# Kernel optimization log

Hardware: AMD Instinct MI355X
Metric: run time of the kernel (lower is better)

## Reference

```python
import jax, jax.numpy as jnp
import numpy as np

N_PROD, N_CUST = 100000, 50000
HID, OUT = 128, 64
E_PP, E_PC, E_LB = 800000, 800000, 400000


def sage(x_src, x_dst, src, dst, Wl, bl, Wr, n_dst):
    # PyG SAGEConv (mean aggr): lin_l(mean_{j->i} x_j) + lin_r(x_i); bias on lin_l only
    msg = x_src[src]                                             # [E, d] gather
    s = jax.ops.segment_sum(msg, dst, num_segments=n_dst)        # [n_dst, d]
    cnt = jax.ops.segment_sum(jnp.ones((src.shape[0],), x_src.dtype), dst, num_segments=n_dst)
    mean = s / jnp.maximum(cnt, 1.0)[:, None]
    return mean @ Wl.T + bl + x_dst @ Wr.T


def setup_inputs() -> dict:
    key = jax.random.key(0)
    ks = iter(jax.random.split(key, 40))

    def lin_w(i, o):
        return (jax.random.normal(next(ks), (o, i), jnp.float32) / np.sqrt(i))

    inp = {}
    inp['x_product'] = jax.random.normal(next(ks), (N_PROD, HID), jnp.float32)
    inp['x_customer'] = jax.random.normal(next(ks), (N_CUST, HID), jnp.float32)
    inp['ei_pp'] = jax.random.randint(next(ks), (2, E_PP), 0, N_PROD)
    src_pc = jax.random.randint(next(ks), (1, E_PC), 0, N_PROD)
    dst_pc = jax.random.randint(next(ks), (1, E_PC), 0, N_CUST)
    inp['ei_pc'] = jnp.concatenate([src_pc, dst_pc], axis=0)
    row = jax.random.randint(next(ks), (1, E_LB), 0, N_CUST)
    col = jax.random.randint(next(ks), (1, E_LB), 0, N_PROD)
    inp['edge_label_index'] = jnp.concatenate([row, col], axis=0)

    # ItemGNNEncoder params
    inp['it_W1l'], inp['it_W1r'] = lin_w(HID, HID), lin_w(HID, HID)
    inp['it_b1'] = jnp.zeros((HID,), jnp.float32)
    inp['it_W2l'], inp['it_W2r'] = lin_w(HID, HID), lin_w(HID, HID)
    inp['it_b2'] = jnp.zeros((HID,), jnp.float32)
    inp['it_Wlin'] = lin_w(HID, OUT)
    inp['it_blin'] = jnp.zeros((OUT,), jnp.float32)
    # UserGNNEncoder params
    inp['us_W1l'], inp['us_W1r'] = lin_w(HID, HID), lin_w(HID, HID)
    inp['us_b1'] = jnp.zeros((HID,), jnp.float32)
    inp['us_W2l'], inp['us_W2r'] = lin_w(HID, HID), lin_w(HID, HID)
    inp['us_b2'] = jnp.zeros((HID,), jnp.float32)
    inp['us_W3l'], inp['us_W3r'] = lin_w(HID, HID), lin_w(HID, HID)
    inp['us_b3'] = jnp.zeros((HID,), jnp.float32)
    inp['us_Wlin'] = lin_w(HID, OUT)
    inp['us_blin'] = jnp.zeros((OUT,), jnp.float32)
    # EdgeDecoder params
    inp['de_W1'] = lin_w(2 * OUT, OUT)
    inp['de_b1'] = jnp.zeros((OUT,), jnp.float32)
    inp['de_W2'] = lin_w(OUT, 1)
    inp['de_b2'] = jnp.zeros((1,), jnp.float32)
    return inp


def reference(x_product, x_customer, ei_pp, ei_pc, edge_label_index,
              it_W1l, it_b1, it_W1r, it_W2l, it_b2, it_W2r, it_Wlin, it_blin,
              us_W1l, us_b1, us_W1r, us_W2l, us_b2, us_W2r, us_W3l, us_b3, us_W3r,
              us_Wlin, us_blin, de_W1, de_b1, de_W2, de_b2):
    pp_s, pp_d = ei_pp[0], ei_pp[1]
    pc_s, pc_d = ei_pc[0], ei_pc[1]

    # ItemGNNEncoder on product-product metapath
    p = jax.nn.relu(sage(x_product, x_product, pp_s, pp_d, it_W1l, it_b1, it_W1r, N_PROD))
    p = jax.nn.relu(sage(p, p, pp_s, pp_d, it_W2l, it_b2, it_W2r, N_PROD))
    z_prod = p @ it_Wlin.T + it_blin                              # [N_PROD, OUT]

    # UserGNNEncoder
    px = jax.nn.relu(sage(x_product, x_product, pp_s, pp_d, us_W1l, us_b1, us_W1r, N_PROD))
    cx = jax.nn.relu(sage(x_product, x_customer, pc_s, pc_d, us_W2l, us_b2, us_W2r, N_CUST))
    cx = jax.nn.relu(sage(px, cx, pc_s, pc_d, us_W3l, us_b3, us_W3r, N_CUST))
    z_cust = cx @ us_Wlin.T + us_blin                             # [N_CUST, OUT]

    # EdgeDecoder: gather-concat-MLP
    row, col = edge_label_index[0], edge_label_index[1]
    z = jnp.concatenate([z_cust[row], z_prod[col]], axis=-1)      # [E_LB, 2*OUT]
    z = jax.nn.relu(z @ de_W1.T + de_b1)
    return z @ de_W2.T + de_b2                                    # [E_LB, 1]
```

## Files before the change

kernel.cpp:

```cpp
#include <hip/hip_runtime.h>
#include <hip/hip_bf16.h>

#define HID   128
#define OUTD  64
#define NPROD 100000
#define NCUST 50000
#define EPP   800000
#define EPC   800000
#define ELB   400000
#define NBK   391
#define EBLK  4096
#define RCAP3 512
#define BCAP3 2560
#define CPADN 400
#define NB3   392
#define NCAST 6250

typedef __bf16 bf16x8 __attribute__((ext_vector_type(8)));
typedef float  f32x4  __attribute__((ext_vector_type(4)));
typedef unsigned short u16;
typedef unsigned int u32;

__device__ __forceinline__ float b2f(u16 u) {
  unsigned int v = ((unsigned int)u) << 16;
  float f; __builtin_memcpy(&f, &v, 4); return f;
}
__device__ __forceinline__ u16 f2b(float f) {
  __hip_bfloat16 h = __float2bfloat16(f);
  u16 u; __builtin_memcpy(&u, &h, 2); return u;
}

union Pack8 { u16 u[8]; int4 v; };

__device__ __forceinline__ int sidx(int row, int chunk) {
  return row * HID + ((chunk ^ (row & 15)) << 3);
}
__device__ __forceinline__ int sidx64(int row, int chunk) {
  return row * 64 + ((chunk ^ (row & 7)) << 3);
}

#define NJOBS 13
struct CastJobs { const float* src[NJOBS]; int n8[NJOBS]; };

__global__ __launch_bounds__(256) void k_prep(const int* __restrict__ ei_pp,
                                              const int* __restrict__ ei_pc,
                                              int* __restrict__ bfill_pp,
                                              int* __restrict__ bfill_pc,
                                              u32* __restrict__ bss_pp,
                                              u32* __restrict__ bss_pc,
                                              const float* __restrict__ x_prod,
                                              u16* __restrict__ XPB,
                                              CastJobs jobs,
                                              u16* __restrict__ wbuf) {
  __shared__ int lcnt[NBK], lstart[NBK], lfill[NBK], gbase[NBK];
  __shared__ u32 spay[EBLK];
  __shared__ u16 sbk[EBLK];
  __shared__ int wtot[4];
  const int t = threadIdx.x;
  int bid = blockIdx.x;

  if (bid >= NB3) {
    bid -= NB3;
    if (bid < NCAST) {
      int i = bid * 256 + t;
      float4 a = ((const float4*)x_prod)[2 * i];
      float4 b = ((const float4*)x_prod)[2 * i + 1];
      Pack8 p;
      p.u[0] = f2b(a.x); p.u[1] = f2b(a.y); p.u[2] = f2b(a.z); p.u[3] = f2b(a.w);
      p.u[4] = f2b(b.x); p.u[5] = f2b(b.y); p.u[6] = f2b(b.z); p.u[7] = f2b(b.w);
      ((int4*)XPB)[i] = p.v;
      return;
    }
    bid -= NCAST;
    int job = bid >> 3;
    int idx = (bid & 7) * 256 + t;
    int off8 = (job < 10) ? job * 2048 : 10 * 2048 + (job - 10) * 1024;
    if (idx >= jobs.n8[job]) return;
    const float* s = jobs.src[job];
    float4 a = ((const float4*)s)[2 * idx];
    float4 b = ((const float4*)s)[2 * idx + 1];
    Pack8 p;
    p.u[0] = f2b(a.x); p.u[1] = f2b(a.y); p.u[2] = f2b(a.z); p.u[3] = f2b(a.w);
    p.u[4] = f2b(b.x); p.u[5] = f2b(b.y); p.u[6] = f2b(b.z); p.u[7] = f2b(b.w);
    ((int4*)wbuf)[off8 + idx] = p.v;
    return;
  }

  const int lane = t & 63, wv = t >> 6;
  int xcc; asm("s_getreg_b32 %0, hwreg(HW_REG_XCC_ID)" : "=s"(xcc));
  const int rep = xcc & 7;
  const int NBLK_PP = (EPP + EBLK - 1) / EBLK;
  const bool isPP = bid < NBLK_PP;
  const int* ei = isPP ? ei_pp : ei_pc;
  const int E  = isPP ? EPP : EPC;
  const int SH = isPP ? 8 : 7;
  int* bfill = isPP ? bfill_pp : bfill_pc;
  u32* bss   = isPP ? bss_pp : bss_pc;
  const int base = (isPP ? bid : bid - NBLK_PP) * EBLK;
  const int n = min(EBLK, E - base);

  for (int j = t; j < NBK; j += 256) { lcnt[j] = 0; lfill[j] = 0; }
  __syncthreads();

  u32 pay[16]; int bk[16];
  const int e0 = t * 16;
  const int* srcp = ei + base;
  const int* dstp = ei + E + base;
  #pragma unroll
  for (int i = 0; i < 16; ++i) bk[i] = -1;
  if (e0 < n) {
    #pragma unroll
    for (int i = 0; i < 4; ++i) {
      int4 s4 = *(const int4*)(srcp + e0 + i * 4);
      int4 d4 = *(const int4*)(dstp + e0 + i * 4);
      int ss[4] = {s4.x, s4.y, s4.z, s4.w};
      int dd[4] = {d4.x, d4.y, d4.z, d4.w};
      #pragma unroll
      for (int j = 0; j < 4; ++j) {
        int b = dd[j] >> SH;
        bk[i * 4 + j] = b;
        pay[i * 4 + j] = ((u32)ss[j] << SH) | (u32)(dd[j] & ((1 << SH) - 1));
        atomicAdd(&lcnt[b], 1);
      }
    }
  }
  __syncthreads();
  {
    int a0 = (2 * t < NBK) ? lcnt[2 * t] : 0;
    int a1 = (2 * t + 1 < NBK) ? lcnt[2 * t + 1] : 0;
    int s = a0 + a1;
    #pragma unroll
    for (int d = 1; d < 64; d <<= 1) {
      int u = __shfl_up(s, d, 64);
      if (lane >= d) s += u;
    }
    if (lane == 63) wtot[wv] = s;
    __syncthreads();
    int wpre = 0;
    for (int w = 0; w < wv; ++w) wpre += wtot[w];
    int excl = s + wpre - (a0 + a1);
    if (2 * t < NBK) lstart[2 * t] = excl;
    if (2 * t + 1 < NBK) lstart[2 * t + 1] = excl + a0;
  }
  __syncthreads();
  for (int b = t; b < NBK; b += 256) {
    int c = lcnt[b];
    gbase[b] = c ? atomicAdd(&bfill[(rep * CPADN + b) << 4], c) : 0;
  }
  #pragma unroll
  for (int i = 0; i < 16; ++i) {
    if (bk[i] >= 0) {
      int pos = lstart[bk[i]] + atomicAdd(&lfill[bk[i]], 1);
      spay[pos] = pay[i];
      sbk[pos] = (u16)bk[i];
    }
  }
  __syncthreads();
  for (int i = t; i < n; i += 256) {
    int b = sbk[i];
    int slot = gbase[b] + (i - lstart[b]);
    if (slot < RCAP3)
      bss[(b * 8 + rep) * RCAP3 + slot] = spay[i];
  }
}

__global__ __launch_bounds__(256) void k_bsort2(const u32* __restrict__ bss_pp,
                                                const int* __restrict__ bfill_pp,
                                                const u32* __restrict__ bss_pc,
                                                const int* __restrict__ bfill_pc,
                                                int* __restrict__ gctr,
                                                int* __restrict__ esrc_pp,
                                                int* __restrict__ start_pp,
                                                int* __restrict__ cnt_pp,
                                                int* __restrict__ esrc_pc,
                                                int* __restrict__ start_pc,
                                                int* __restrict__ cnt_pc) {
  __shared__ u32 pairs[BCAP3];
  __shared__ int outsrc[BCAP3];
  __shared__ int lcnt[256], lstart[256], lfill[256];
  __shared__ int sh_n, sh_base, rn[8], roff[8], wtot[4];
  const int tid = threadIdx.x;
  const int lane = tid & 63, wv = tid >> 6;
  const bool isPP = (int)blockIdx.x < NBK;
  const int b = isPP ? (int)blockIdx.x : (int)blockIdx.x - NBK;
  const int K   = isPP ? 256 : 128;
  const int SHL = isPP ? 8 : 7;
  const u32* bss   = isPP ? bss_pp : bss_pc;
  const int* bfill = isPP ? bfill_pp : bfill_pc;
  int* gc    = isPP ? gctr : gctr + 1;
  int* esrc  = isPP ? esrc_pp : esrc_pc;
  int* start = isPP ? start_pp : start_pc;
  int* cnt   = isPP ? cnt_pp : cnt_pc;
  const int n_nodes = isPP ? NPROD : NCUST;

  if (tid < 8) rn[tid] = min(bfill[(tid * CPADN + b) << 4], RCAP3);
  for (int j = tid; j < K; j += 256) { lcnt[j] = 0; lfill[j] = 0; }
  __syncthreads();
  if (tid == 0) {
    int run = 0;
    for (int r = 0; r < 8; ++r) {
      roff[r] = run;
      int m = min(rn[r], BCAP3 - run);
      rn[r] = m;
      run += m;
    }
    sh_n = run;
    sh_base = atomicAdd(gc, run);
  }
  __syncthreads();
  const int n = sh_n, base = sh_base;
  const int Km1 = K - 1;
  #pragma unroll
  for (int r = 0; r < 8; ++r) {
    int m = rn[r], o = roff[r];
    for (int i = tid; i < m; i += 256) {
      u32 p = bss[(b * 8 + r) * RCAP3 + i];
      pairs[o + i] = p;
      atomicAdd(&lcnt[p & Km1], 1);
    }
  }
  __syncthreads();
  {
    int a0 = (2 * tid < K) ? lcnt[2 * tid] : 0;
    int a1 = (2 * tid + 1 < K) ? lcnt[2 * tid + 1] : 0;
    int s = a0 + a1;
    #pragma unroll
    for (int d = 1; d < 64; d <<= 1) {
      int u = __shfl_up(s, d, 64);
      if (lane >= d) s += u;
    }
    if (lane == 63) wtot[wv] = s;
    __syncthreads();
    int wpre = 0;
    for (int w = 0; w < wv; ++w) wpre += wtot[w];
    int excl = s + wpre - (a0 + a1);
    if (2 * tid < K) lstart[2 * tid] = excl;
    if (2 * tid + 1 < K) lstart[2 * tid + 1] = excl + a0;
  }
  __syncthreads();
  for (int i = tid; i < n; i += 256) {
    u32 p = pairs[i];
    int ln = p & Km1;
    int pos = lstart[ln] + atomicAdd(&lfill[ln], 1);
    outsrc[pos] = (int)(p >> SHL);
  }
  __syncthreads();
  for (int i = tid; i < n; i += 256) esrc[base + i] = outsrc[i];
  const int nb0 = b * K;
  for (int j = tid; j < K; j += 256) {
    int g = nb0 + j;
    if (g < n_nodes) { start[g] = base + lstart[j]; cnt[g] = lcnt[j]; }
  }
}

__global__ __launch_bounds__(256) void k_agg2(const int* __restrict__ es_a,
                                              const int* __restrict__ st_a,
                                              const int* __restrict__ cn_a,
                                              const u16* __restrict__ xa,
                                              u16* __restrict__ oa, int na,
                                              const int* __restrict__ es_b,
                                              const int* __restrict__ st_b,
                                              const int* __restrict__ cn_b,
                                              const u16* __restrict__ xb,
                                              u16* __restrict__ ob, int nb, int blkA) {
  const int t = threadIdx.x;
  const bool A = (int)blockIdx.x < blkA;
  const int node = (A ? (int)blockIdx.x : (int)blockIdx.x - blkA) * 16 + (t >> 4);
  const int l16 = t & 15;
  const int q4  = t & 48;
  if (node >= (A ? na : nb)) return;
  const int* esrc  = A ? es_a : es_b;
  const u16* x     = A ? xa : xb;
  u16* outm        = A ? oa : ob;
  int s0 = (A ? st_a : st_b)[node];
  int c  = (A ? cn_a : cn_b)[node];
  float acc[8] = {0.f, 0.f, 0.f, 0.f, 0.f, 0.f, 0.f, 0.f};
  for (int j0 = 0; j0 < c; j0 += 16) {
    int nch = min(16, c - j0);
    int eid = (l16 < nch) ? esrc[s0 + j0 + l16] : 0;
    int k = 0;
    for (; k + 4 <= nch; k += 4) {
      int s0i = __shfl(eid, q4 + k, 64);
      int s1i = __shfl(eid, q4 + k + 1, 64);
      int s2i = __shfl(eid, q4 + k + 2, 64);
      int s3i = __shfl(eid, q4 + k + 3, 64);
      Pack8 p0, p1, p2, p3;
      p0.v = *(const int4*)(x + (size_t)s0i * HID + l16 * 8);
      p1.v = *(const int4*)(x + (size_t)s1i * HID + l16 * 8);
      p2.v = *(const int4*)(x + (size_t)s2i * HID + l16 * 8);
      p3.v = *(const int4*)(x + (size_t)s3i * HID + l16 * 8);
      #pragma unroll
      for (int u = 0; u < 8; ++u)
        acc[u] += (b2f(p0.u[u]) + b2f(p1.u[u])) + (b2f(p2.u[u]) + b2f(p3.u[u]));
    }
    for (; k < nch; ++k) {
      int s = __shfl(eid, q4 + k, 64);
      Pack8 p;
      p.v = *(const int4*)(x + (size_t)s * HID + l16 * 8);
      #pragma unroll
      for (int u = 0; u < 8; ++u) acc[u] += b2f(p.u[u]);
    }
  }
  float inv = 1.0f / (float)max(c, 1);
  Pack8 o;
  #pragma unroll
  for (int u = 0; u < 8; ++u) o.u[u] = f2b(acc[u] * inv);
  *(int4*)(outm + (size_t)node * HID + l16 * 8) = o.v;
}

__global__ __launch_bounds__(256) void k_lay1(
    const u16* __restrict__ cxA1, const u16* __restrict__ cxW1,
    const float* __restrict__ cxA2f, const u16* __restrict__ cxW2,
    const float* __restrict__ cxBias, u16* __restrict__ cxOut, int Mcx,
    const u16* __restrict__ A1, const u16* __restrict__ A2,
    const u16* __restrict__ Wa, const u16* __restrict__ Wb,
    const u16* __restrict__ Wc, const u16* __restrict__ Wd,
    const float* __restrict__ bias1, const float* __restrict__ bias2,
    u16* __restrict__ out1, u16* __restrict__ out2, int M2o,
    int blkCx) {
  __shared__ __align__(16) u16 sA1[64 * HID];
  __shared__ __align__(16) u16 sA2[64 * HID];
  __shared__ __align__(16) u16 sW[128 * HID];
  const int tid  = threadIdx.x;
  const int lane = tid & 63;
  const int wave = tid >> 6;
  const int q    = lane >> 4;
  const int r16  = lane & 15;
  const bool isCx = (int)blockIdx.x < blkCx;

  if (isCx) {
    const int m0 = blockIdx.x * 64;
    f32x4 acc[4][2];
    #pragma unroll
    for (int i = 0; i < 4; ++i)
      #pragma unroll
      for (int j = 0; j < 2; ++j) {
        acc[i][j][0] = 0.f; acc[i][j][1] = 0.f; acc[i][j][2] = 0.f; acc[i][j][3] = 0.f;
      }
    #pragma unroll
    for (int phase = 0; phase < 2; ++phase) {
      const u16* W = phase ? cxW2 : cxW1;
      if (phase) __syncthreads();
      #pragma unroll
      for (int i = 0; i < 4; ++i) {
        int idx = i * 256 + tid;
        int rr = idx >> 4, c8 = idx & 15;
        int gr = m0 + rr;
        Pack8 p; p.v = make_int4(0, 0, 0, 0);
        if (gr < Mcx) {
          if (phase == 0) {
            p.v = *(const int4*)(cxA1 + (size_t)gr * HID + c8 * 8);
          } else {
            const float* s = cxA2f + (size_t)gr * HID + c8 * 8;
            float4 f0 = ((const float4*)s)[0], f1 = ((const float4*)s)[1];
            p.u[0] = f2b(f0.x); p.u[1] = f2b(f0.y); p.u[2] = f2b(f0.z); p.u[3] = f2b(f0.w);
            p.u[4] = f2b(f1.x); p.u[5] = f2b(f1.y); p.u[6] = f2b(f1.z); p.u[7] = f2b(f1.w);
          }
        }
        *(int4*)(sA1 + sidx(rr, c8)) = p.v;
      }
      #pragma unroll
      for (int i = 0; i < 8; ++i) {
        int idx = i * 256 + tid;
        int rr = idx >> 4, c8 = idx & 15;
        *(int4*)(sW + sidx(rr, c8)) = *(const int4*)(W + (size_t)rr * HID + c8 * 8);
      }
      __syncthreads();
      #pragma unroll
      for (int ks = 0; ks < 4; ++ks) {
        int chunk = ks * 4 + q;
        bf16x8 a[4], b[2];
        #pragma unroll
        for (int mi = 0; mi < 4; ++mi)
          a[mi] = *(const bf16x8*)(sA1 + sidx(mi * 16 + r16, chunk));
        #pragma unroll
        for (int ni = 0; ni < 2; ++ni)
          b[ni] = *(const bf16x8*)(sW + sidx(wave * 32 + ni * 16 + r16, chunk));
        #pragma unroll
        for (int mi = 0; mi < 4; ++mi)
          #pragma unroll
          for (int ni = 0; ni < 2; ++ni)
            acc[mi][ni] = __builtin_amdgcn_mfma_f32_16x16x32_bf16(a[mi], b[ni], acc[mi][ni], 0, 0, 0);
      }
    }
    #pragma unroll
    for (int ni = 0; ni < 2; ++ni) {
      int col = wave * 32 + ni * 16 + r16;
      float bv = cxBias[col];
      #pragma unroll
      for (int mi = 0; mi < 4; ++mi)
        #pragma unroll
        for (int r = 0; r < 4; ++r) {
          int gr = m0 + mi * 16 + q * 4 + r;
          if (gr < Mcx)
            cxOut[(size_t)gr * HID + col] = f2b(fmaxf(acc[mi][ni][r] + bv, 0.f));
        }
    }
    return;
  }

  const int m0 = ((int)blockIdx.x - blkCx) * 64;
  f32x4 acc1[4][2], acc2[4][2];
  #pragma unroll
  for (int i = 0; i < 4; ++i)
    #pragma unroll
    for (int j = 0; j < 2; ++j) {
      acc1[i][j][0] = 0.f; acc1[i][j][1] = 0.f; acc1[i][j][2] = 0.f; acc1[i][j][3] = 0.f;
      acc2[i][j][0] = 0.f; acc2[i][j][1] = 0.f; acc2[i][j][2] = 0.f; acc2[i][j][3] = 0.f;
    }

  #pragma unroll
  for (int i = 0; i < 4; ++i) {
    int idx = i * 256 + tid;
    int rr = idx >> 4, c8 = idx & 15;
    int gr = m0 + rr;
    Pack8 p1, p2;
    p1.v = make_int4(0, 0, 0, 0);
    p2.v = make_int4(0, 0, 0, 0);
    if (gr < M2o) {
      p1.v = *(const int4*)(A1 + (size_t)gr * HID + c8 * 8);
      p2.v = *(const int4*)(A2 + (size_t)gr * HID + c8 * 8);
    }
    *(int4*)(sA1 + sidx(rr, c8)) = p1.v;
    *(int4*)(sA2 + sidx(rr, c8)) = p2.v;
  }

  bf16x8 af[4][4];

  auto stageW = [&](const u16* W) {
    #pragma unroll
    for (int i = 0; i < 8; ++i) {
      int idx = i * 256 + tid;
      int rr = idx >> 4, c8 = idx & 15;
      *(int4*)(sW + sidx(rr, c8)) = *(const int4*)(W + (size_t)rr * HID + c8 * 8);
    }
  };
  auto loadA = [&](const u16* sA) {
    #pragma unroll
    for (int ks = 0; ks < 4; ++ks)
      #pragma unroll
      for (int mi = 0; mi < 4; ++mi)
        af[ks][mi] = *(const bf16x8*)(sA + sidx(mi * 16 + r16, ks * 4 + q));
  };
  auto mf = [&](f32x4 (&acc)[4][2]) {
    #pragma unroll
    for (int ks = 0; ks < 4; ++ks) {
      int chunk = ks * 4 + q;
      bf16x8 b[2];
      #pragma unroll
      for (int ni = 0; ni < 2; ++ni)
        b[ni] = *(const bf16x8*)(sW + sidx(wave * 32 + ni * 16 + r16, chunk));
      #pragma unroll
      for (int mi = 0; mi < 4; ++mi)
        #pragma unroll
        for (int ni = 0; ni < 2; ++ni)
          acc[mi][ni] = __builtin_amdgcn_mfma_f32_16x16x32_bf16(af[ks][mi], b[ni], acc[mi][ni], 0, 0, 0);
    }
  };

  stageW(Wa);
  __syncthreads();
  loadA(sA1);
  mf(acc1);
  __syncthreads();
  stageW(Wc);
  __syncthreads();
  mf(acc2);
  __syncthreads();
  stageW(Wb);
  __syncthreads();
  loadA(sA2);
  mf(acc1);
  __syncthreads();
  stageW(Wd);
  __syncthreads();
  mf(acc2);

  #pragma unroll
  for (int ni = 0; ni < 2; ++ni) {
    int col = wave * 32 + ni * 16 + r16;
    float bv1 = bias1[col];
    float bv2 = bias2[col];
    #pragma unroll
    for (int mi = 0; mi < 4; ++mi)
      #pragma unroll
      for (int r = 0; r < 4; ++r) {
        int gr = m0 + mi * 16 + q * 4 + r;
        if (gr < M2o) {
          out1[(size_t)gr * HID + col] = f2b(fmaxf(acc1[mi][ni][r] + bv1, 0.f));
          out2[(size_t)gr * HID + col] = f2b(fmaxf(acc2[mi][ni][r] + bv2, 0.f));
        }
      }
  }
}

__global__ __launch_bounds__(256) void k_chain2(
    const u16* __restrict__ A1a, const u16* __restrict__ W1a,
    const u16* __restrict__ A2a, const u16* __restrict__ W2a,
    const float* __restrict__ biasa, u16* __restrict__ outa, int Ma,
    const u16* __restrict__ Wlina, const float* __restrict__ blina,
    const u16* __restrict__ dW1a, const float* __restrict__ db1a,
    const u16* __restrict__ A1b, const u16* __restrict__ W1b,
    const u16* __restrict__ A2b, const u16* __restrict__ W2b,
    const float* __restrict__ biasb, u16* __restrict__ outb, int Mb,
    const u16* __restrict__ Wlinb, const float* __restrict__ blinb,
    const u16* __restrict__ dW1b, const float* __restrict__ db1b,
    int blkA) {
  __shared__ __align__(16) u16 sA[64 * HID];
  __shared__ __align__(16) u16 sW[128 * HID];
  const bool isA = (int)blockIdx.x < blkA;
  const u16* A1 = isA ? A1a : A1b;
  const u16* W1 = isA ? W1a : W1b;
  const u16* A2 = isA ? A2a : A2b;
  const u16* W2 = isA ? W2a : W2b;
  const float* bias = isA ? biasa : biasb;
  u16* out = isA ? outa : outb;
  const int M = isA ? Ma : Mb;
  const u16* Wlin = isA ? Wlina : Wlinb;
  const float* blin = isA ? blina : blinb;
  const u16* dW1 = isA ? dW1a : dW1b;
  const float* db1 = isA ? db1a : db1b;

  const int tid  = threadIdx.x;
  const int lane = tid & 63;
  const int wave = tid >> 6;
  const int q    = lane >> 4;
  const int r16  = lane & 15;
  const int m0   = (isA ? (int)blockIdx.x : (int)blockIdx.x - blkA) * 64;

  f32x4 acc[4][2];
  #pragma unroll
  for (int i = 0; i < 4; ++i)
    #pragma unroll
    for (int j = 0; j < 2; ++j) {
      acc[i][j][0] = 0.f; acc[i][j][1] = 0.f; acc[i][j][2] = 0.f; acc[i][j][3] = 0.f;
    }

  #pragma unroll
  for (int phase = 0; phase < 2; ++phase) {
    const u16* W = phase ? W2 : W1;
    const u16* A = phase ? A2 : A1;
    if (phase) __syncthreads();
    #pragma unroll
    for (int i = 0; i < 4; ++i) {
      int idx = i * 256 + tid;
      int rr = idx >> 4, c8 = idx & 15;
      int gr = m0 + rr;
      Pack8 p; p.v = make_int4(0, 0, 0, 0);
      if (gr < M) p.v = *(const int4*)(A + (size_t)gr * HID + c8 * 8);
      *(int4*)(sA + sidx(rr, c8)) = p.v;
    }
    #pragma unroll
    for (int i = 0; i < 8; ++i) {
      int idx = i * 256 + tid;
      int rr = idx >> 4, c8 = idx & 15;
      *(int4*)(sW + sidx(rr, c8)) = *(const int4*)(W + (size_t)rr * HID + c8 * 8);
    }
    __syncthreads();
    #pragma unroll
    for (int ks = 0; ks < 4; ++ks) {
      int chunk = ks * 4 + q;
      bf16x8 a[4], b[2];
      #pragma unroll
      for (int mi = 0; mi < 4; ++mi)
        a[mi] = *(const bf16x8*)(sA + sidx(mi * 16 + r16, chunk));
      #pragma unroll
      for (int ni = 0; ni < 2; ++ni)
        b[ni] = *(const bf16x8*)(sW + sidx(wave * 32 + ni * 16 + r16, chunk));
      #pragma unroll
      for (int mi = 0; mi < 4; ++mi)
        #pragma unroll
        for (int ni = 0; ni < 2; ++ni)
          acc[mi][ni] = __builtin_amdgcn_mfma_f32_16x16x32_bf16(a[mi], b[ni], acc[mi][ni], 0, 0, 0);
    }
  }

  __syncthreads();
  #pragma unroll
  for (int ni = 0; ni < 2; ++ni) {
    int col = wave * 32 + ni * 16 + r16;
    float bv = bias[col];
    #pragma unroll
    for (int mi = 0; mi < 4; ++mi)
      #pragma unroll
      for (int r = 0; r < 4; ++r) {
        int rl = mi * 16 + q * 4 + r;
        float v = fmaxf(acc[mi][ni][r] + bv, 0.f);
        sA[rl * HID + (((col >> 3) ^ (rl & 15)) << 3) + (col & 7)] = f2b(v);
      }
  }
  #pragma unroll
  for (int i = 0; i < 4; ++i) {
    int idx = i * 256 + tid;
    int rr = idx >> 4, c8 = idx & 15;
    *(int4*)(sW + sidx(rr, c8)) = *(const int4*)(Wlin + (size_t)rr * HID + c8 * 8);
  }
  #pragma unroll
  for (int i = 0; i < 2; ++i) {
    int idx = i * 256 + tid;
    int rr = idx >> 3, c8 = idx & 7;
    *(int4*)(sW + 8192 + sidx64(rr, c8)) = *(const int4*)(dW1 + (size_t)rr * HID + c8 * 8);
  }
  __syncthreads();
  f32x4 az[4];
  #pragma unroll
  for (int i = 0; i < 4; ++i) { az[i][0]=0.f; az[i][1]=0.f; az[i][2]=0.f; az[i][3]=0.f; }
  #pragma unroll
  for (int ks = 0; ks < 4; ++ks) {
    int chunk = ks * 4 + q;
    bf16x8 b = *(const bf16x8*)(sW + sidx(wave * 16 + r16, chunk));
    #pragma unroll
    for (int mi = 0; mi < 4; ++mi) {
      bf16x8 a = *(const bf16x8*)(sA + sidx(mi * 16 + r16, chunk));
      az[mi] = __builtin_amdgcn_mfma_f32_16x16x32_bf16(a, b, az[mi], 0, 0, 0);
    }
  }
  {
    int col = wave * 16 + r16;
    float bl = blin[col];
    #pragma unroll
    for (int mi = 0; mi < 4; ++mi)
      #pragma unroll
      for (int r = 0; r < 4; ++r) {
        int rl = mi * 16 + q * 4 + r;
        sW[12288 + rl * 64 + (((col >> 3) ^ (rl & 7)) << 3) + (col & 7)] = f2b(az[mi][r] + bl);
      }
  }
  __syncthreads();
  f32x4 au[4];
  #pragma unroll
  for (int i = 0; i < 4; ++i) { au[i][0]=0.f; au[i][1]=0.f; au[i][2]=0.f; au[i][3]=0.f; }
  #pragma unroll
  for (int ks = 0; ks < 2; ++ks) {
    int chunk = ks * 4 + q;
    bf16x8 b = *(const bf16x8*)(sW + 8192 + sidx64(wave * 16 + r16, chunk));
    #pragma unroll
    for (int mi = 0; mi < 4; ++mi) {
      bf16x8 a = *(const bf16x8*)(sW + 12288 + sidx64(mi * 16 + r16, chunk));
      au[mi] = __builtin_amdgcn_mfma_f32_16x16x32_bf16(a, b, au[mi], 0, 0, 0);
    }
  }
  {
    int col = wave * 16 + r16;
    float db = db1 ? db1[col] : 0.f;
    #pragma unroll
    for (int mi = 0; mi < 4; ++mi)
      #pragma unroll
      for (int r = 0; r < 4; ++r) {
        int gr = m0 + mi * 16 + q * 4 + r;
        if (gr < M) out[(size_t)gr * 64 + col] = f2b(au[mi][r] + db);
      }
  }
}

__global__ __launch_bounds__(256) void k_edge(const u16* __restrict__ U,
                                              const u16* __restrict__ V,
                                              const int* __restrict__ eli,
                                              const float* __restrict__ w2,
                                              const float* __restrict__ b2,
                                              float* __restrict__ out) {
  const int lane = threadIdx.x & 63;
  const int wave = threadIdx.x >> 6;
  const int se   = (lane >> 3);
  const int ch   = lane & 7;
  float w2c[8];
  #pragma unroll
  for (int j = 0; j < 8; ++j) w2c[j] = w2[ch * 8 + j];
  const float b2v = b2[0];
  const int e0 = blockIdx.x * 256;
  #pragma unroll
  for (int p = 0; p < 8; ++p) {
    int e = e0 + p * 32 + wave * 8 + se;
    if (e < ELB) {
      int r = eli[e];
      int c = eli[ELB + e];
      Pack8 pu, pv;
      pu.v = *(const int4*)(U + (size_t)r * 64 + ch * 8);
      pv.v = *(const int4*)(V + (size_t)c * 64 + ch * 8);
      float s = 0.f;
      #pragma unroll
      for (int j = 0; j < 8; ++j)
        s += fmaxf(b2f(pu.u[j]) + b2f(pv.u[j]), 0.f) * w2c[j];
      s += __shfl_xor(s, 1, 64);
      s += __shfl_xor(s, 2, 64);
      s += __shfl_xor(s, 4, 64);
      if (ch == 0) out[e] = s + b2v;
    }
  }
}

extern "C" void kernel_launch(void* const* d_in, const int* in_sizes, int n_in,
                              void* d_out, int out_size, void* d_ws, size_t ws_size,
                              hipStream_t stream) {
  const float* x_prod = (const float*)d_in[0];
  const float* x_cust = (const float*)d_in[1];
  const int* ei_pp    = (const int*)d_in[2];
  const int* ei_pc    = (const int*)d_in[3];
  const int* eli      = (const int*)d_in[4];

  const float *it_W1l, *it_W1r, *it_b1, *it_W2l, *it_W2r, *it_b2, *it_Wlin, *it_blin;
  const float *us_W1l, *us_W1r, *us_b1, *us_W2l, *us_W2r, *us_b2;
  const float *us_W3l, *us_W3r, *us_b3, *us_Wlin, *us_blin;
  if (in_sizes[6] == 128) {
    it_W1l  = (const float*)d_in[5];  it_b1   = (const float*)d_in[6];  it_W1r  = (const float*)d_in[7];
    it_W2l  = (const float*)d_in[8];  it_b2   = (const float*)d_in[9];  it_W2r  = (const float*)d_in[10];
    it_Wlin = (const float*)d_in[11]; it_blin = (const float*)d_in[12];
    us_W1l  = (const float*)d_in[13]; us_b1   = (const float*)d_in[14]; us_W1r  = (const float*)d_in[15];
    us_W2l  = (const float*)d_in[16]; us_b2   = (const float*)d_in[17]; us_W2r  = (const float*)d_in[18];
    us_W3l  = (const float*)d_in[19]; us_b3   = (const float*)d_in[20]; us_W3r  = (const float*)d_in[21];
    us_Wlin = (const float*)d_in[22]; us_blin = (const float*)d_in[23];
  } else {
    it_W1l  = (const float*)d_in[5];  it_W1r  = (const float*)d_in[6];  it_b1   = (const float*)d_in[7];
    it_W2l  = (const float*)d_in[8];  it_W2r  = (const float*)d_in[9];  it_b2   = (const float*)d_in[10];
    it_Wlin = (const float*)d_in[11]; it_blin = (const float*)d_in[12];
    us_W1l  = (const float*)d_in[13]; us_W1r  = (const float*)d_in[14]; us_b1   = (const float*)d_in[15];
    us_W2l  = (const float*)d_in[16]; us_W2r  = (const float*)d_in[17]; us_b2   = (const float*)d_in[18];
    us_W3l  = (const float*)d_in[19]; us_W3r  = (const float*)d_in[20]; us_b3   = (const float*)d_in[21];
    us_Wlin = (const float*)d_in[22]; us_blin = (const float*)d_in[23];
  }
  const float* de_W1 = (const float*)d_in[24];
  const float* de_b1 = (const float*)d_in[25];
  const float* de_W2 = (const float*)d_in[26];
  const float* de_b2 = (const float*)d_in[27];

  char* ws = (char*)d_ws;
  int* bfill_pp = (int*)(ws + 0);
  int* bfill_pc = (int*)(ws + 409600);
  int* gctr     = (int*)(ws + 819200);
  int* start_pp = (int*)(ws + 819264);
  int* cnt_pp   = (int*)(ws + 1219264);
  int* start_pc = (int*)(ws + 1619264);
  int* cnt_pc   = (int*)(ws + 1819264);
  int* esrc_pp  = (int*)(ws + 2019264);
  int* esrc_pc  = (int*)(ws + 5219264);
  u16* wbuf  = (u16*)(ws + 8419264);
  u16* XPB   = (u16*)(ws + 8796096);
  u16* meanb = (u16*)(ws + 34396096);
  u16* P1    = (u16*)(ws + 59996096);
  u16* meanc = (u16*)(ws + 85596096);
  u16* CX    = (u16*)(ws + 98396096);
  u32* bss_pp = (u32*)P1;
  u32* bss_pc = (u32*)(ws + 59996096 + 6553600);
  u16* PX = XPB;
  u16* U  = (u16*)esrc_pp;
  u16* V  = CX;

  u16* w_it1l = wbuf + 0 * 16384;  u16* w_it1r = wbuf + 1 * 16384;
  u16* w_it2l = wbuf + 2 * 16384;  u16* w_it2r = wbuf + 3 * 16384;
  u16* w_us1l = wbuf + 4 * 16384;  u16* w_us1r = wbuf + 5 * 16384;
  u16* w_us2l = wbuf + 6 * 16384;  u16* w_us2r = wbuf + 7 * 16384;
  u16* w_us3l = wbuf + 8 * 16384;  u16* w_us3r = wbuf + 9 * 16384;
  u16* w_itlin = wbuf + 10 * 16384;
  u16* w_uslin = wbuf + 10 * 16384 + 8192;
  u16* w_deW1  = wbuf + 10 * 16384 + 2 * 8192;

  (void)n_in; (void)out_size; (void)ws_size;

  hipMemsetAsync(d_ws, 0, 819208, stream);

  dim3 B(256);
  CastJobs jobs;
  jobs.src[0] = it_W1l;  jobs.src[1] = it_W1r;  jobs.src[2] = it_W2l;  jobs.src[3] = it_W2r;
  jobs.src[4] = us_W1l;  jobs.src[5] = us_W1r;  jobs.src[6] = us_W2l;  jobs.src[7] = us_W2r;
  jobs.src[8] = us_W3l;  jobs.src[9] = us_W3r;
  jobs.src[10] = it_Wlin; jobs.src[11] = us_Wlin; jobs.src[12] = de_W1;
  for (int i = 0; i < 10; ++i) jobs.n8[i] = 2048;
  for (int i = 10; i < 13; ++i) jobs.n8[i] = 1024;

  k_prep<<<dim3(NB3 + NCAST + NJOBS * 8), B, 0, stream>>>(
      ei_pp, ei_pc, bfill_pp, bfill_pc, bss_pp, bss_pc, x_prod, XPB, jobs, wbuf);
  k_bsort2<<<dim3(2 * NBK), B, 0, stream>>>(bss_pp, bfill_pp, bss_pc, bfill_pc, gctr,
                                            esrc_pp, start_pp, cnt_pp,
                                            esrc_pc, start_pc, cnt_pc);

  const int HALF = 50000;
  const int GH = HALF / 16;
  dim3 Gc((NCUST + 63) / 64);

  k_agg2<<<dim3(GH), B, 0, stream>>>(esrc_pp, start_pp, cnt_pp, XPB, meanb, HALF,
                                     esrc_pp, start_pp, cnt_pp, XPB, meanb, 0, GH);
  k_agg2<<<dim3(GH), B, 0, stream>>>(esrc_pp, start_pp + HALF, cnt_pp + HALF, XPB,
                                     meanb + (size_t)HALF * HID, HALF,
                                     esrc_pp, start_pp, cnt_pp, XPB, meanb, 0, GH);
  k_agg2<<<dim3(GH), B, 0, stream>>>(esrc_pc, start_pc, cnt_pc, XPB, meanc, NCUST,
                                     esrc_pc, start_pc, cnt_pc, XPB, meanc, 0, GH);
  k_lay1<<<dim3(782 + 1563), B, 0, stream>>>(
      meanc, w_us2l, x_cust, w_us2r, us_b2, CX, NCUST,
      meanb, XPB, w_it1l, w_it1r, w_us1l, w_us1r,
      it_b1, us_b1, P1, PX, NPROD, 782);
  k_agg2<<<dim3(GH), B, 0, stream>>>(esrc_pp, start_pp, cnt_pp, P1, meanb, HALF,
                                     esrc_pp, start_pp, cnt_pp, P1, meanb, 0, GH);
  k_agg2<<<dim3(GH), B, 0, stream>>>(esrc_pp, start_pp + HALF, cnt_pp + HALF, P1,
                                     meanb + (size_t)HALF * HID, HALF,
                                     esrc_pp, start_pp, cnt_pp, P1, meanb, 0, GH);
  k_agg2<<<dim3(GH), B, 0, stream>>>(esrc_pc, start_pc, cnt_pc, PX, meanc, NCUST,
                                     esrc_pc, start_pc, cnt_pc, PX, meanc, 0, GH);
  k_chain2<<<dim3(782 + 1563), B, 0, stream>>>(
      meanc, w_us3l, CX, w_us3r, us_b3, U, NCUST, w_uslin, us_blin, w_deW1, de_b1,
      meanb, w_it2l, P1, w_it2r, it_b2, V, NPROD, w_itlin, it_blin, w_deW1 + 64, nullptr,
      782);
  k_edge<<<dim3((ELB + 255) / 256), B, 0, stream>>>(U, V, eli, de_W2, de_b2, (float*)d_out);
}
```

Baseline: 485.9 us.

## Merge aggregation launches and stream second A operand from global

```diff
diff --git a/kernel.cpp b/kernel.cpp
--- a/kernel.cpp
+++ b/kernel.cpp
@@ -38,6 +38,7 @@
 __device__ __forceinline__ int sidx64(int row, int chunk) {
   return row * 64 + ((chunk ^ (row & 7)) << 3);
 }
+
 
 #define NJOBS 13
 struct CastJobs { const float* src[NJOBS]; int n8[NJOBS]; };
@@ -319,7 +320,6 @@
     u16* __restrict__ out1, u16* __restrict__ out2, int M2o,
     int blkCx) {
   __shared__ __align__(16) u16 sA1[64 * HID];
-  __shared__ __align__(16) u16 sA2[64 * HID];
   __shared__ __align__(16) u16 sW[128 * HID];
   const int tid  = threadIdx.x;
   const int lane = tid & 63;
@@ -414,15 +414,9 @@
     int idx = i * 256 + tid;
     int rr = idx >> 4, c8 = idx & 15;
     int gr = m0 + rr;
-    Pack8 p1, p2;
-    p1.v = make_int4(0, 0, 0, 0);
-    p2.v = make_int4(0, 0, 0, 0);
-    if (gr < M2o) {
-      p1.v = *(const int4*)(A1 + (size_t)gr * HID + c8 * 8);
-      p2.v = *(const int4*)(A2 + (size_t)gr * HID + c8 * 8);
-    }
+    Pack8 p1; p1.v = make_int4(0, 0, 0, 0);
+    if (gr < M2o) p1.v = *(const int4*)(A1 + (size_t)gr * HID + c8 * 8);
     *(int4*)(sA1 + sidx(rr, c8)) = p1.v;
-    *(int4*)(sA2 + sidx(rr, c8)) = p2.v;
   }
 
   bf16x8 af[4][4];
@@ -435,12 +429,24 @@
       *(int4*)(sW + sidx(rr, c8)) = *(const int4*)(W + (size_t)rr * HID + c8 * 8);
     }
   };
-  auto loadA = [&](const u16* sA) {
+  auto loadA1 = [&]() {
     #pragma unroll
     for (int ks = 0; ks < 4; ++ks)
       #pragma unroll
       for (int mi = 0; mi < 4; ++mi)
-        af[ks][mi] = *(const bf16x8*)(sA + sidx(mi * 16 + r16, ks * 4 + q));
+        af[ks][mi] = *(const bf16x8*)(sA1 + sidx(mi * 16 + r16, ks * 4 + q));
+  };
+  auto loadA2g = [&]() {
+    #pragma unroll
+    for (int ks = 0; ks < 4; ++ks)
+      #pragma unroll
+      for (int mi = 0; mi < 4; ++mi) {
+        int gr = m0 + mi * 16 + r16;
+        union { int4 v; bf16x8 b; } p;
+        p.v = make_int4(0, 0, 0, 0);
+        if (gr < M2o) p.v = *(const int4*)(A2 + (size_t)gr * HID + (ks * 4 + q) * 8);
+        af[ks][mi] = p.b;
+      }
   };
   auto mf = [&](f32x4 (&acc)[4][2]) {
     #pragma unroll
@@ -460,16 +466,16 @@
 
   stageW(Wa);
   __syncthreads();
-  loadA(sA1);
+  loadA1();
   mf(acc1);
   __syncthreads();
   stageW(Wc);
   __syncthreads();
   mf(acc2);
+  loadA2g();
   __syncthreads();
   stageW(Wb);
   __syncthreads();
-  loadA(sA2);
   mf(acc1);
   __syncthreads();
   stageW(Wd);
@@ -773,28 +779,17 @@
                                             esrc_pp, start_pp, cnt_pp,
                                             esrc_pc, start_pc, cnt_pc);
 
-  const int HALF = 50000;
-  const int GH = HALF / 16;
-  dim3 Gc((NCUST + 63) / 64);
-
-  k_agg2<<<dim3(GH), B, 0, stream>>>(esrc_pp, start_pp, cnt_pp, XPB, meanb, HALF,
-                                     esrc_pp, start_pp, cnt_pp, XPB, meanb, 0, GH);
-  k_agg2<<<dim3(GH), B, 0, stream>>>(esrc_pp, start_pp + HALF, cnt_pp + HALF, XPB,
-                                     meanb + (size_t)HALF * HID, HALF,
-                                     esrc_pp, start_pp, cnt_pp, XPB, meanb, 0, GH);
-  k_agg2<<<dim3(GH), B, 0, stream>>>(esrc_pc, start_pc, cnt_pc, XPB, meanc, NCUST,
-                                     esrc_pc, start_pc, cnt_pc, XPB, meanc, 0, GH);
+  dim3 Gp((NPROD + 63) / 64), Gc((NCUST + 63) / 64);
+  const int App = (NPROD + 15) / 16, Apc = (NCUST + 15) / 16;
+
+  k_agg2<<<dim3(App + Apc), B, 0, stream>>>(esrc_pp, start_pp, cnt_pp, XPB, meanb, NPROD,
+                                            esrc_pc, start_pc, cnt_pc, XPB, meanc, NCUST, App);
   k_lay1<<<dim3(782 + 1563), B, 0, stream>>>(
       meanc, w_us2l, x_cust, w_us2r, us_b2, CX, NCUST,
       meanb, XPB, w_it1l, w_it1r, w_us1l, w_us1r,
       it_b1, us_b1, P1, PX, NPROD, 782);
-  k_agg2<<<dim3(GH), B, 0, stream>>>(esrc_pp, start_pp, cnt_pp, P1, meanb, HALF,
-                                     esrc_pp, start_pp, cnt_pp, P1, meanb, 0, GH);
-  k_agg2<<<dim3(GH), B, 0, stream>>>(esrc_pp, start_pp + HALF, cnt_pp + HALF, P1,
-                                     meanb + (size_t)HALF * HID, HALF,
-                                     esrc_pp, start_pp, cnt_pp, P1, meanb, 0, GH);
-  k_agg2<<<dim3(GH), B, 0, stream>>>(esrc_pc, start_pc, cnt_pc, PX, meanc, NCUST,
-                                     esrc_pc, start_pc, cnt_pc, PX, meanc, 0, GH);
+  k_agg2<<<dim3(App + Apc), B, 0, stream>>>(esrc_pp, start_pp, cnt_pp, P1, meanb, NPROD,
+                                            esrc_pc, start_pc, cnt_pc, PX, meanc, NCUST, App);
   k_chain2<<<dim3(782 + 1563), B, 0, stream>>>(
       meanc, w_us3l, CX, w_us3r, us_b3, U, NCUST, w_uslin, us_blin, w_deW1, de_b1,
       meanb, w_it2l, P1, w_it2r, it_b2, V, NPROD, w_itlin, it_blin, w_deW1 + 64, nullptr,
```

After: 477.0 us, median of 2. Within noise of the previous version (-1.8%).
